# Performance work log

Hardware: AMD Instinct MI355X
Metric: run time of the kernel (lower is better)

Reference implementation:

```python
import jax, jax.numpy as jnp
import numpy as np
import math

B, IN, OUT = 32, 8192, 8192
DENSITY = 0.15

def _inverse_softplus(v):
    return math.log(math.expm1(v))

def setup_inputs() -> dict:
    key = jax.random.key(0)
    k1, k2, k3, k4 = jax.random.split(key, 4)
    inputs = jax.random.normal(k1, (B, IN), dtype=jnp.float32)
    active = jax.random.uniform(k2, (OUT, IN)) < DENSITY
    sign = jnp.where(jax.random.uniform(k3, (OUT, IN)) < 0.5, 1, -1)
    weight_state = jnp.where(active, sign, 0).astype(jnp.int32)
    # log_scale initialized so softplus(log_scale) = 1/sqrt(in_features)
    log_scale = jnp.full((OUT,), _inverse_softplus(1.0 / math.sqrt(IN)), dtype=jnp.float32)
    bias = jax.random.normal(k4, (OUT,), dtype=jnp.float32) * 0.01
    return {"inputs": inputs, "log_scale": log_scale, "bias": bias, "weight_state": weight_state}

def reference(inputs, log_scale, bias, weight_state):
    # scale = softplus(log_scale).clamp_min(1e-4), per output channel
    scale = jnp.maximum(jax.nn.softplus(log_scale), 1e-4)  # [OUT]
    # effective_weight = ternary_state * scale[:, None]; out = x @ W^T + b
    w = weight_state.astype(inputs.dtype) * scale[:, None]  # [OUT, IN]
    return jnp.einsum('bi,oi->bo', inputs, w) + bias
```

## Files before the change

kernel.cpp:

```cpp
#include <hip/hip_runtime.h>
#include <hip/hip_bf16.h>
#include <cmath>


#define K_SZ   8192
#define N_SZ   8192
#define B_SZ   32
#define KSPLIT 8
#define KSPAN  (K_SZ / KSPLIT)
#define BK     128
#define STEPS  (KSPAN / BK)
#define BN     64
#define LDB    136

typedef __attribute__((ext_vector_type(8))) short bf16x8;
typedef __attribute__((ext_vector_type(4))) float f32x4;

__device__ __forceinline__ unsigned pack_rn(float lo, float hi) {
  unsigned ul = __builtin_bit_cast(unsigned, lo) + 0x8000u;
  unsigned uh = __builtin_bit_cast(unsigned, hi) + 0x8000u;
  return (ul >> 16) | (uh & 0xFFFF0000u);
}
__device__ __forceinline__ unsigned pack_w(int w0, int w1) {
  unsigned u0 = __builtin_bit_cast(unsigned, (float)w0);
  unsigned u1 = __builtin_bit_cast(unsigned, (float)w1);
  return (u0 >> 16) | (u1 & 0xFFFF0000u);
}

__global__ void xprep(const float* __restrict__ X, uint4* __restrict__ Xr) {
  int t = blockIdx.x * blockDim.x + threadIdx.x;
  int lane = t & 63;
  int chunk = t >> 6;
  int kb = chunk >> 1;
  int mt = chunk & 1;
  int row = mt * 16 + (lane & 15);
  int k0 = kb * 32 + (lane >> 4) * 8;
  const float* p = X + (size_t)row * K_SZ + k0;
  float4 a = *(const float4*)p;
  float4 b = *(const float4*)(p + 4);
  uint4 o;
  o.x = pack_rn(a.x, a.y); o.y = pack_rn(a.z, a.w);
  o.z = pack_rn(b.x, b.y); o.w = pack_rn(b.z, b.w);
  Xr[t] = o;
}

__global__ __launch_bounds__(256, 4) void tmm(
    const int*   __restrict__ W,
    const uint4* __restrict__ Xr,
    const float* __restrict__ log_scale,
    const float* __restrict__ bias,
    float*       __restrict__ out) {
  __shared__ unsigned short lds[4][16 * LDB];

  const int tid  = threadIdx.x;
  const int w    = tid >> 6;
  const int lane = tid & 63;
  const int q    = lane >> 4;
  const int r    = lane & 15;
  const int nb   = blockIdx.x * BN;
  const int kh   = blockIdx.y;

  const int srow = lane >> 5;
  const int skof = 4 * (lane & 31);
  const int* gW = W + (size_t)(nb + w * 16 + srow) * K_SZ + (size_t)kh * KSPAN + skof;
  unsigned short* lw = &lds[w][0];
  const int wofs = srow * LDB + skof;

  int4 wr[8];
  #pragma unroll
  for (int j = 0; j < 8; ++j) wr[j] = *(const int4*)(gW + (size_t)j * 2 * K_SZ);

  f32x4 acc0 = {0.f,0.f,0.f,0.f};
  f32x4 acc1 = {0.f,0.f,0.f,0.f};
  const int rb = r * LDB;
  const int kb_blk = kh * (KSPAN / 32);

  for (int step = 0; step < STEPS; ++step) {
    uint2 p[8];
    #pragma unroll
    for (int j = 0; j < 8; ++j) {
      p[j].x = pack_w(wr[j].x, wr[j].y);
      p[j].y = pack_w(wr[j].z, wr[j].w);
    }
    if (step + 1 < STEPS) {
      const int* g = gW + (step + 1) * BK;
      #pragma unroll
      for (int j = 0; j < 8; ++j) wr[j] = *(const int4*)(g + (size_t)j * 2 * K_SZ);
    }
    #pragma unroll
    for (int j = 0; j < 8; ++j)
      *(uint2*)&lw[wofs + j * 2 * LDB] = p[j];

    const int kb0 = kb_blk + step * 4;
    uint4 am[4][2];
    #pragma unroll
    for (int s = 0; s < 4; ++s) {
      am[s][0] = Xr[(size_t)((kb0 + s) * 2 + 0) * 64 + lane];
      am[s][1] = Xr[(size_t)((kb0 + s) * 2 + 1) * 64 + lane];
    }

    #pragma unroll
    for (int s = 0; s < 4; ++s) {
      bf16x8 Bf = *(const bf16x8*)&lw[rb + s * 32 + q * 8];
      acc0 = __builtin_amdgcn_mfma_f32_16x16x32_bf16(
                 __builtin_bit_cast(bf16x8, am[s][0]), Bf, acc0, 0, 0, 0);
      acc1 = __builtin_amdgcn_mfma_f32_16x16x32_bf16(
                 __builtin_bit_cast(bf16x8, am[s][1]), Bf, acc1, 0, 0, 0);
    }
  }

  const int o = nb + w * 16 + r;
  float sp    = log1pf(expf(log_scale[o]));
  float scale = fmaxf(sp, 1e-4f);
  float badd  = (kh == 0) ? bias[o] : 0.f;
  #pragma unroll
  for (int rg = 0; rg < 4; ++rg) {
    int b0 = q * 4 + rg;
    atomicAdd(&out[(size_t)b0 * N_SZ + o],        acc0[rg] * scale + badd);
    atomicAdd(&out[(size_t)(b0 + 16) * N_SZ + o], acc1[rg] * scale + badd);
  }
}

extern "C" void kernel_launch(void* const* d_in, const int* in_sizes, int n_in,
                              void* d_out, int out_size, void* d_ws, size_t ws_size,
                              hipStream_t stream) {
  const float* X  = (const float*)d_in[0];
  const float* ls = (const float*)d_in[1];
  const float* bs = (const float*)d_in[2];
  const int*   W  = (const int*)d_in[3];
  float* out = (float*)d_out;
  uint4* Xr = (uint4*)d_ws;

  hipMemsetAsync(out, 0, (size_t)B_SZ * N_SZ * sizeof(float), stream);
  xprep<<<128, 256, 0, stream>>>(X, Xr);
  dim3 grid(N_SZ / BN, KSPLIT);
  tmm<<<grid, 256, 0, stream>>>(W, Xr, ls, bs, out);
}
```

Baseline: 387.5 us.

## Stream weights via global_load_lds double buffer and replace atomics with partial-sum reduce

Weight tiles now go from global memory straight into LDS through the global_load_lds DMA builtin, using an XOR-swizzled layout and double buffering. The int-to-bf16 conversion moves to after the LDS read. The split-K atomicAdd epilogue and the memset are replaced by plain stores of per-split partial sums into workspace, followed by a separate reduce kernel that applies softplus scale and bias. This removes register staging and atomic contention. In exchange it adds an extra kernel launch and roughly 8 MB of partial-sum traffic, and the kernel's launch bounds drop to 3 blocks per multiprocessor.

```diff
diff --git a/kernel.cpp b/kernel.cpp
--- a/kernel.cpp
+++ b/kernel.cpp
@@ -8,10 +8,8 @@
 #define B_SZ   32
 #define KSPLIT 8
 #define KSPAN  (K_SZ / KSPLIT)
-#define BK     128
-#define STEPS  (KSPAN / BK)
+#define NHALF  16
 #define BN     64
-#define LDB    136
 
 typedef __attribute__((ext_vector_type(8))) short bf16x8;
 typedef __attribute__((ext_vector_type(4))) float f32x4;
@@ -25,6 +23,12 @@
   unsigned u0 = __builtin_bit_cast(unsigned, (float)w0);
   unsigned u1 = __builtin_bit_cast(unsigned, (float)w1);
   return (u0 >> 16) | (u1 & 0xFFFF0000u);
+}
+
+__device__ __forceinline__ void dma16(const int* g, int* l) {
+  __builtin_amdgcn_global_load_lds(
+      (const __attribute__((address_space(1))) unsigned*)g,
+      (__attribute__((address_space(3))) unsigned*)l, 16, 0, 0);
 }
 
 __global__ void xprep(const float* __restrict__ X, uint4* __restrict__ Xr) {
@@ -44,13 +48,11 @@
   Xr[t] = o;
 }
 
-__global__ __launch_bounds__(256, 4) void tmm(
+__global__ __launch_bounds__(256, 3) void tmm(
     const int*   __restrict__ W,
     const uint4* __restrict__ Xr,
-    const float* __restrict__ log_scale,
-    const float* __restrict__ bias,
-    float*       __restrict__ out) {
-  __shared__ unsigned short lds[4][16 * LDB];
+    float*       __restrict__ part) {
+  __shared__ int lds[4][2][1024];
 
   const int tid  = threadIdx.x;
   const int w    = tid >> 6;
@@ -59,66 +61,79 @@
   const int r    = lane & 15;
   const int nb   = blockIdx.x * BN;
   const int kh   = blockIdx.y;
+  const int lh   = lane >> 4, l15 = lane & 15;
 
-  const int srow = lane >> 5;
-  const int skof = 4 * (lane & 31);
-  const int* gW = W + (size_t)(nb + w * 16 + srow) * K_SZ + (size_t)kh * KSPAN + skof;
-  unsigned short* lw = &lds[w][0];
-  const int wofs = srow * LDB + skof;
+  const int* gp[4];
+  #pragma unroll
+  for (int j = 0; j < 4; ++j) {
+    int rp = j * 4 + lh;
+    int c  = l15 ^ rp;
+    gp[j] = W + (size_t)(nb + w * 16 + rp) * K_SZ + (size_t)kh * KSPAN + c * 4;
+  }
+  #pragma unroll
+  for (int j = 0; j < 4; ++j) dma16(gp[j], &lds[w][0][j * 256]);
 
-  int4 wr[8];
+  const int kbb = kh * (KSPAN / 32);
+  uint4 am[2][4];
   #pragma unroll
-  for (int j = 0; j < 8; ++j) wr[j] = *(const int4*)(gW + (size_t)j * 2 * K_SZ);
+  for (int s = 0; s < 2; ++s) {
+    am[0][s * 2 + 0] = Xr[(size_t)((kbb + s) * 2 + 0) * 64 + lane];
+    am[0][s * 2 + 1] = Xr[(size_t)((kbb + s) * 2 + 1) * 64 + lane];
+  }
 
-  f32x4 acc0 = {0.f,0.f,0.f,0.f};
-  f32x4 acc1 = {0.f,0.f,0.f,0.f};
-  const int rb = r * LDB;
-  const int kb_blk = kh * (KSPAN / 32);
+  f32x4 acc0 = {0.f, 0.f, 0.f, 0.f};
+  f32x4 acc1 = {0.f, 0.f, 0.f, 0.f};
 
-  for (int step = 0; step < STEPS; ++step) {
-    uint2 p[8];
+  #pragma unroll 2
+  for (int h = 0; h < NHALF; ++h) {
+    const int cb = h & 1, nbuf = cb ^ 1;
+    if (h + 1 < NHALF) {
+      #pragma unroll
+      for (int j = 0; j < 4; ++j) dma16(gp[j] + (h + 1) * 64, &lds[w][nbuf][j * 256]);
+      const int kb2 = kbb + (h + 1) * 2;
+      #pragma unroll
+      for (int s = 0; s < 2; ++s) {
+        am[nbuf][s * 2 + 0] = Xr[(size_t)((kb2 + s) * 2 + 0) * 64 + lane];
+        am[nbuf][s * 2 + 1] = Xr[(size_t)((kb2 + s) * 2 + 1) * 64 + lane];
+      }
+    }
+    const int* buf = &lds[w][cb][0];
     #pragma unroll
-    for (int j = 0; j < 8; ++j) {
-      p[j].x = pack_w(wr[j].x, wr[j].y);
-      p[j].y = pack_w(wr[j].z, wr[j].w);
-    }
-    if (step + 1 < STEPS) {
-      const int* g = gW + (step + 1) * BK;
-      #pragma unroll
-      for (int j = 0; j < 8; ++j) wr[j] = *(const int4*)(g + (size_t)j * 2 * K_SZ);
-    }
-    #pragma unroll
-    for (int j = 0; j < 8; ++j)
-      *(uint2*)&lw[wofs + j * 2 * LDB] = p[j];
-
-    const int kb0 = kb_blk + step * 4;
-    uint4 am[4][2];
-    #pragma unroll
-    for (int s = 0; s < 4; ++s) {
-      am[s][0] = Xr[(size_t)((kb0 + s) * 2 + 0) * 64 + lane];
-      am[s][1] = Xr[(size_t)((kb0 + s) * 2 + 1) * 64 + lane];
-    }
-
-    #pragma unroll
-    for (int s = 0; s < 4; ++s) {
-      bf16x8 Bf = *(const bf16x8*)&lw[rb + s * 32 + q * 8];
+    for (int s = 0; s < 2; ++s) {
+      const int c0 = s * 8 + q * 2;
+      int4 lo = *(const int4*)&buf[(r * 16 + ((c0)     ^ r)) * 4];
+      int4 hi = *(const int4*)&buf[(r * 16 + ((c0 + 1) ^ r)) * 4];
+      union { unsigned u[4]; bf16x8 v; } Bf;
+      Bf.u[0] = pack_w(lo.x, lo.y); Bf.u[1] = pack_w(lo.z, lo.w);
+      Bf.u[2] = pack_w(hi.x, hi.y); Bf.u[3] = pack_w(hi.z, hi.w);
       acc0 = __builtin_amdgcn_mfma_f32_16x16x32_bf16(
-                 __builtin_bit_cast(bf16x8, am[s][0]), Bf, acc0, 0, 0, 0);
+                 __builtin_bit_cast(bf16x8, am[cb][s * 2 + 0]), Bf.v, acc0, 0, 0, 0);
       acc1 = __builtin_amdgcn_mfma_f32_16x16x32_bf16(
-                 __builtin_bit_cast(bf16x8, am[s][1]), Bf, acc1, 0, 0, 0);
+                 __builtin_bit_cast(bf16x8, am[cb][s * 2 + 1]), Bf.v, acc1, 0, 0, 0);
     }
   }
 
   const int o = nb + w * 16 + r;
-  float sp    = log1pf(expf(log_scale[o]));
-  float scale = fmaxf(sp, 1e-4f);
-  float badd  = (kh == 0) ? bias[o] : 0.f;
+  float* pb = part + (size_t)kh * B_SZ * N_SZ + o;
   #pragma unroll
   for (int rg = 0; rg < 4; ++rg) {
-    int b0 = q * 4 + rg;
-    atomicAdd(&out[(size_t)b0 * N_SZ + o],        acc0[rg] * scale + badd);
-    atomicAdd(&out[(size_t)(b0 + 16) * N_SZ + o], acc1[rg] * scale + badd);
+    pb[(size_t)(q * 4 + rg) * N_SZ]        = acc0[rg];
+    pb[(size_t)(16 + q * 4 + rg) * N_SZ]   = acc1[rg];
   }
+}
+
+__global__ void reduce_k(const float* __restrict__ part,
+                         const float* __restrict__ ls,
+                         const float* __restrict__ bias,
+                         float* __restrict__ out) {
+  int idx = blockIdx.x * 256 + threadIdx.x;
+  int o = idx & (N_SZ - 1);
+  float s = 0.f;
+  #pragma unroll
+  for (int kh = 0; kh < KSPLIT; ++kh)
+    s += part[(size_t)kh * B_SZ * N_SZ + idx];
+  float sp = log1pf(expf(ls[o]));
+  out[idx] = s * fmaxf(sp, 1e-4f) + bias[o];
 }
 
 extern "C" void kernel_launch(void* const* d_in, const int* in_sizes, int n_in,
@@ -128,11 +143,12 @@
   const float* ls = (const float*)d_in[1];
   const float* bs = (const float*)d_in[2];
   const int*   W  = (const int*)d_in[3];
-  float* out = (float*)d_out;
-  uint4* Xr = (uint4*)d_ws;
+  float* out  = (float*)d_out;
+  uint4* Xr   = (uint4*)d_ws;
+  float* part = (float*)((char*)d_ws + (512 << 10));
 
-  hipMemsetAsync(out, 0, (size_t)B_SZ * N_SZ * sizeof(float), stream);
   xprep<<<128, 256, 0, stream>>>(X, Xr);
   dim3 grid(N_SZ / BN, KSPLIT);
-  tmm<<<grid, 256, 0, stream>>>(W, Xr, ls, bs, out);
+  tmm<<<grid, 256, 0, stream>>>(W, Xr, part);
+  reduce_k<<<(B_SZ * N_SZ) / 256, 256, 0, stream>>>(part, ls, bs, out);
 }
```

Measured after the change: 412.2 us. 1.06x slower.
